# Performance work log

Hardware: AMD Instinct MI355X
Metric: run time of the kernel (lower is better)

Reference implementation:

```python
import jax, jax.numpy as jnp
import numpy as np

EPS = 1e-5  # torch GroupNorm default
KNN_K = 16


def _knn_idx(Q, P, K):
    # Q:[B,Nq,3], P:[B,Np,3] -> idx [B,Nq,K], ascending squared distance
    d = (jnp.sum(Q * Q, -1)[:, :, None] + jnp.sum(P * P, -1)[:, None, :]
         - 2.0 * jnp.einsum('bqc,bkc->bqk', Q, P))
    _, idx = jax.lax.top_k(-d, K)
    return idx


def _gather_nbr(feat_bnc, idx_bqk):
    # feat:[B,Np,C], idx:[B,Nq,K] -> [B,Nq,K,C]  (knn_gather)
    return jax.vmap(lambda f, i: f[i])(feat_bnc, idx_bqk)


def _group_norm(x_bcnk, gamma, beta, num_groups=8):
    B, C, N, K = x_bcnk.shape
    G = min(num_groups, C)
    xg = x_bcnk.reshape(B, G, C // G, N, K)
    mu = xg.mean(axis=(2, 3, 4), keepdims=True)
    var = xg.var(axis=(2, 3, 4), keepdims=True)
    xn = ((xg - mu) / jnp.sqrt(var + EPS)).reshape(B, C, N, K)
    return xn * gamma[None, :, None, None] + beta[None, :, None, None]


def _edge_conv(Fq_bcn, Fk_bcn, Pq_b3n, Pk_b3n, k, W, gamma, beta):
    # EdgeConv: concat(x_j - x_i, x_i) -> conv1x1 -> GN -> ReLU -> max over K
    idx = _knn_idx(Pq_b3n.transpose(0, 2, 1), Pk_b3n.transpose(0, 2, 1), k)
    nbr = _gather_nbr(Fk_bcn.transpose(0, 2, 1), idx)          # [B,Nq,K,Cin]
    Fi = jnp.broadcast_to(Fq_bcn.transpose(0, 2, 1)[:, :, None, :], nbr.shape)
    pair = jnp.concatenate([nbr - Fi, Fi], axis=-1)            # [B,Nq,K,2Cin]
    out = jnp.einsum('oc,bnkc->bonk', W, pair)                 # conv 1x1, no bias
    out = _group_norm(out, gamma, beta)
    out = jax.nn.relu(out)
    return out.max(axis=-1)                                    # [B,Cout,Nq]


def _fps_idx(P_b3n, m):
    # Farthest point sampling starting at index 0 (pytorch3d default)
    def one(Pn3):
        d0 = jnp.sum((Pn3 - Pn3[0]) ** 2, -1)
        def step(dists, _):
            nxt = jnp.argmax(dists)
            d = jnp.sum((Pn3 - Pn3[nxt]) ** 2, -1)
            return jnp.minimum(dists, d), nxt
        _, idxs = jax.lax.scan(step, d0, None, length=m - 1)
        return jnp.concatenate([jnp.zeros((1,), jnp.int32), idxs.astype(jnp.int32)])
    return jax.vmap(one)(P_b3n.transpose(0, 2, 1))


def _gather_bcn(x_bcn, idx_bm):
    return jax.vmap(lambda x, i: x[:, i])(x_bcn, idx_bm)


def setup_inputs() -> dict:
    key = jax.random.key(0)
    ks = jax.random.split(key, 8)
    B, N = 2, 8192
    def w(k, shape, s=0.1):
        return jax.random.normal(k, shape, jnp.float32) * s
    return {
        'xyz': jax.random.normal(ks[0], (B, 3, N), jnp.float32),
        'stem_w': w(ks[1], (8, 3)), 'stem_b': jnp.zeros((8,), jnp.float32),
        'w1': w(ks[2], (32, 16)),  'g1': jnp.ones((32,), jnp.float32),  'b1': jnp.zeros((32,), jnp.float32),
        'w2': w(ks[3], (64, 64)),  'g2': jnp.ones((64,), jnp.float32),  'b2': jnp.zeros((64,), jnp.float32),
        'w3': w(ks[4], (64, 128)), 'g3': jnp.ones((64,), jnp.float32),  'b3': jnp.zeros((64,), jnp.float32),
        'w4': w(ks[5], (128, 128)),'g4': jnp.ones((128,), jnp.float32), 'b4': jnp.zeros((128,), jnp.float32),
    }


def reference(xyz, stem_w, stem_b, w1, g1, b1, w2, g2, b2, w3, g3, b3, w4, g4, b4):
    K = KNN_K
    P0 = xyz                                                     # [B,3,N0]
    F0 = jnp.einsum('oc,bcn->bon', stem_w, xyz) + stem_b[None, :, None]
    F0a = _edge_conv(F0, F0, P0, P0, K, w1, g1, b1)              # [B,32,N0]
    N0 = P0.shape[2]
    N1 = max(1, N0 // 4)
    idx1 = _fps_idx(P0, N1)
    P1 = _gather_bcn(P0, idx1)
    F1sk = _gather_bcn(F0a, idx1)
    F1a = _edge_conv(F1sk, F0a, P1, P0, K, w2, g2, b2)           # [B,64,N1]
    N2 = max(1, N1 // 4)
    idx2 = _fps_idx(P1, N2)
    P2 = _gather_bcn(P1, idx2)
    F2sk = _gather_bcn(F1a, idx2)
    F2mid = _edge_conv(F2sk, F1a, P2, P1, K, w3, g3, b3)         # [B,64,N2]
    F2a = _edge_conv(F2mid, F1a, P2, P1, K, w4, g4, b4)          # [B,128,N2]
    return (P0, F0a, P1, F1a, P2, F2a)
```

## Files before the change

### kernel.cpp

```cpp
#include <hip/hip_runtime.h>
#include <math.h>

typedef unsigned long long ull;

__global__ __launch_bounds__(256) void stem_fused(const float* __restrict__ xyz,
    const float* __restrict__ w, const float* __restrict__ bias,
    float* __restrict__ F0, float* __restrict__ P0o, int N){
  int id = blockIdx.x*256 + threadIdx.x;
  int n = id % N; int b = id / N;
  float x = xyz[((size_t)b*3+0)*N+n];
  float y = xyz[((size_t)b*3+1)*N+n];
  float z = xyz[((size_t)b*3+2)*N+n];
  P0o[((size_t)b*3+0)*N+n] = x;
  P0o[((size_t)b*3+1)*N+n] = y;
  P0o[((size_t)b*3+2)*N+n] = z;
  #pragma unroll
  for (int o=0;o<8;o++){
    float v = fmaf(w[o*3+0],x, fmaf(w[o*3+1],y, fmaf(w[o*3+2],z, bias[o])));
    F0[((size_t)b*8+o)*N+n] = v;
  }
}

__global__ __launch_bounds__(256) void knn_fused(
    const float* __restrict__ Pq, const float* __restrict__ Pp,
    int* __restrict__ idxk, int Nq, int Np){
  __shared__ float4 tile[4][256];
  __shared__ float  pd[16][4][64];
  __shared__ int    pi[16][4][64];
  int t = threadIdx.x, w = t>>6, l = t&63;
  int b = blockIdx.y;
  int qn = blockIdx.x*64 + l;
  const float* Pqb = Pq + (size_t)b*3*Nq;
  const float* Ppb = Pp + (size_t)b*3*Np;
  float qx = Pqb[qn], qy = Pqb[Nq+qn], qz = Pqb[2*Nq+qn];
  float qq = __fadd_rn(__fadd_rn(__fmul_rn(qx,qx),__fmul_rn(qy,qy)),__fmul_rn(qz,qz));

  float dl[16]; int il[16];
  #pragma unroll
  for (int u=0;u<16;u++){ dl[u]=INFINITY; il[u]=-1; }
  float maxd = INFINITY; int maxslot = 0;

  int CANDS = Np >> 2;
  int c0 = w*CANDS;
  for (int tb=0; tb<CANDS; tb+=256){
    __syncthreads();
    #pragma unroll
    for (int k=0;k<4;k++){
      int p = c0 + tb + k*64 + l;
      float px = Ppb[p], py = Ppb[Np+p], pz = Ppb[2*Np+p];
      float pp = __fadd_rn(__fadd_rn(__fmul_rn(px,px),__fmul_rn(py,py)),__fmul_rn(pz,pz));
      tile[w][k*64+l] = make_float4(px,py,pz,pp);
    }
    __syncthreads();
    for (int j=0;j<256;j++){
      float4 c = tile[w][j];
      float dot = __fadd_rn(__fadd_rn(__fmul_rn(qx,c.x),__fmul_rn(qy,c.y)),__fmul_rn(qz,c.z));
      float dc  = __fsub_rn(__fadd_rn(qq,c.w), __fmul_rn(2.0f,dot));
      if (dc < maxd){
        int pidx = c0 + tb + j;
        #pragma unroll
        for (int u=0;u<16;u++){ bool sel=(maxslot==u); dl[u]=sel?dc:dl[u]; il[u]=sel?pidx:il[u]; }
        maxd = dl[0]; maxslot = 0;
        #pragma unroll
        for (int u=1;u<16;u++){ bool g=(dl[u]>maxd); maxd=g?dl[u]:maxd; maxslot=g?u:maxslot; }
      }
    }
  }
  #pragma unroll
  for (int u=0;u<16;u++){ pd[u][w][l]=dl[u]; pi[u][w][l]=il[u]; }
  __syncthreads();
  if (t < 64){
    int q = t;
    float mdl[16]; int mil[16];
    #pragma unroll
    for (int u=0;u<16;u++){ mdl[u]=INFINITY; mil[u]=0x7fffffff; }
    float mmaxd = INFINITY; int mmaxi = 0x7fffffff; int mslot = 0;
    for (int s=0;s<4;s++){
      #pragma unroll
      for (int u=0;u<16;u++){
        float d = pd[u][s][q]; int ii = pi[u][s][q];
        bool better = (d < mmaxd) || (d == mmaxd && ii < mmaxi);
        if (better){
          #pragma unroll
          for (int v=0;v<16;v++){ bool sel=(mslot==v); mdl[v]=sel?d:mdl[v]; mil[v]=sel?ii:mil[v]; }
          mmaxd = mdl[0]; mmaxi = mil[0]; mslot = 0;
          #pragma unroll
          for (int v=1;v<16;v++){
            bool g = (mdl[v]>mmaxd) || (mdl[v]==mmaxd && mil[v]>mmaxi);
            mmaxd=g?mdl[v]:mmaxd; mmaxi=g?mil[v]:mmaxi; mslot=g?v:mslot;
          }
        }
      }
    }
    #pragma unroll
    for (int u=0;u<16;u++)
      idxk[((size_t)b*Nq + blockIdx.x*64 + q)*16 + u] = mil[u];
  }
}

template<int CIN, int COUT>
__global__ __launch_bounds__(1024) void edge_conv_pre(
    const float* __restrict__ Fk, const float* __restrict__ Fi,
    const int* __restrict__ idx, const float* __restrict__ W,
    float* __restrict__ pre, float* __restrict__ partS,
    float* __restrict__ partQ, int pstride, int Nq, int Np){
  constexpr int C2  = 2*CIN;
  constexpr int PAD = C2 + 4;
  constexpr int TO  = (COUT <= 64) ? COUT : 64;
  constexpr int OP  = COUT / TO;
  constexpr int CPG = COUT/8;
  constexpr int WPG = CPG/4;
  extern __shared__ float sm[];
  float* Wl = sm;
  float* Pl = sm + COUT*PAD;
  int t = threadIdx.x;
  int n = blockIdx.x, b = blockIdx.y;
  for (int e=t; e<COUT*C2; e += blockDim.x){
    int o=e/C2, c=e%C2; Wl[o*PAD+c] = W[e];
  }
  const int* idxn = idx + ((size_t)b*Nq + n)*16;
  for (int e=t; e<16*C2; e += blockDim.x){
    int k = e/C2, c = e%C2;
    int cc = (c < CIN) ? c : (c-CIN);
    float fi = Fi[((size_t)b*CIN + cc)*Nq + n];
    float v;
    if (c < CIN){ int nb = idxn[k]; v = Fk[((size_t)b*CIN + c)*Np + nb] - fi; }
    else v = fi;
    Pl[k*PAD+c] = v;
  }
  __syncthreads();
  int k = t & 15, o0 = t >> 4;
  float accv[OP];
  #pragma unroll
  for (int op=0; op<OP; op++){
    int o = o0 + op*TO;
    float acc = 0.f;
    #pragma unroll
    for (int c=0;c<C2;c+=4){
      float4 wv = *(const float4*)&Wl[o*PAD+c];
      float4 pv = *(const float4*)&Pl[k*PAD+c];
      acc = fmaf(wv.x,pv.x,acc); acc = fmaf(wv.y,pv.y,acc);
      acc = fmaf(wv.z,pv.z,acc); acc = fmaf(wv.w,pv.w,acc);
    }
    accv[op] = acc;
    pre[(((size_t)b*COUT + o)*Nq + n)*16 + k] = acc;
  }
  int w = t>>6;
  #pragma unroll
  for (int op=0; op<OP; op++){
    float s1 = accv[op], s2 = accv[op]*accv[op];
    #pragma unroll
    for (int off=32; off>=1; off>>=1){ s1 += __shfl_down(s1,off); s2 += __shfl_down(s2,off); }
    if ((t&63)==0){
      int o = o0 + op*TO;
      int g = o / CPG;
      int slot = n*WPG + (w % WPG);
      partS[((size_t)(b*8+g))*pstride + slot] = s1;
      partQ[((size_t)(b*8+g))*pstride + slot] = s2;
    }
  }
}

__global__ __launch_bounds__(256) void gn_combine(const float* __restrict__ partS,
    const float* __restrict__ partQ, float2* __restrict__ stats,
    int nslot, int pstride, double cnt){
  int bg = blockIdx.x, t = threadIdx.x;
  const float* ps = partS + (size_t)bg*pstride;
  const float* pq = partQ + (size_t)bg*pstride;
  double s=0.0, q=0.0;
  for (int i=t; i<nslot; i+=256){ s += (double)ps[i]; q += (double)pq[i]; }
  #pragma unroll
  for (int off=32; off>=1; off>>=1){ s += __shfl_down(s,off); q += __shfl_down(q,off); }
  __shared__ double ls[4], lq[4];
  int wid = t>>6;
  if ((t&63)==0){ ls[wid]=s; lq[wid]=q; }
  __syncthreads();
  if (t==0){
    double S=ls[0]+ls[1]+ls[2]+ls[3], Q=lq[0]+lq[1]+lq[2]+lq[3];
    double mu = S/cnt;
    double var = Q/cnt - mu*mu;
    stats[bg] = make_float2((float)mu, (float)(1.0/sqrt(var+1e-5)));
  }
}

template<int COUT>
__global__ __launch_bounds__(256) void gn_apply(const float* __restrict__ pre,
    const float2* __restrict__ stats, const float* __restrict__ gamma,
    const float* __restrict__ beta, float* __restrict__ outF, int Nq){
  int id = blockIdx.x*256 + threadIdx.x;
  int o = (id/Nq)%COUT; int b = id/(Nq*COUT);
  int g = o/(COUT/8);
  float2 st = stats[b*8+g];
  float muf = st.x, rstd = st.y;
  float ga=gamma[o], be=beta[o];
  const float4* p = (const float4*)(pre + (size_t)id*16);
  float m = 0.f;
  #pragma unroll
  for (int q=0;q<4;q++){
    float4 v = p[q];
    m = fmaxf(m, fmaf((v.x-muf)*rstd, ga, be));
    m = fmaxf(m, fmaf((v.y-muf)*rstd, ga, be));
    m = fmaxf(m, fmaf((v.z-muf)*rstd, ga, be));
    m = fmaxf(m, fmaf((v.w-muf)*rstd, ga, be));
  }
  outF[id] = m;
}

template<int CTRL>
__device__ __forceinline__ float dpp_maxf(float x){
  int y = __builtin_amdgcn_update_dpp(0, __float_as_int(x), CTRL, 0xf, 0xf, true);
  return fmaxf(x, __int_as_float(y));
}

template<int PPT, int BLK, int M>
__global__ __launch_bounds__(BLK, 1) void fps_kernel(const float* __restrict__ P,
    int* __restrict__ idx_out){
  constexpr int N  = PPT*BLK;
  constexpr int NW = BLK/64;
  constexpr int Q  = PPT/4;
  extern __shared__ __align__(16) float sm[];
  float* lx = sm; float* ly = sm+N; float* lz = sm+2*N;
  ull* wk = (ull*)(sm + 3*N);
  int b = blockIdx.x, t = threadIdx.x;
  const float* Pb = P + (size_t)b*3*N;
  for (int i=t; i<N; i+=BLK){ lx[i]=Pb[i]; ly[i]=Pb[N+i]; lz[i]=Pb[2*N+i]; }
  __syncthreads();
  float px[PPT], py[PPT], pz[PPT], dist[PPT];
  #pragma unroll
  for (int j=0;j<PPT;j++){ int p=t*PPT+j; px[j]=lx[p]; py[j]=ly[p]; pz[j]=lz[p]; }
  #pragma unroll
  for (int j=0;j<PPT;j++){
    asm volatile("" : "+v"(px[j]), "+v"(py[j]), "+v"(pz[j]));
  }
  float sx = lx[0], sy = ly[0], sz = lz[0];
  float bd = -1.f; int bj = 0;
  #pragma unroll
  for (int j=0;j<PPT;j++){
    float dx=__fsub_rn(px[j],sx), dy=__fsub_rn(py[j],sy), dz=__fsub_rn(pz[j],sz);
    float dd=__fadd_rn(__fadd_rn(__fmul_rn(dx,dx),__fmul_rn(dy,dy)),__fmul_rn(dz,dz));
    dist[j]=dd;
    bool c = dd > bd; bd = c?dd:bd; bj = c?j:bj;
  }
  int pbest = t*PPT + bj;
  if (t==0) idx_out[(size_t)b*M] = 0;
  int wid = t>>6, lane = t&63, par = 0;
  for (int i=1;i<M;i++){
    float r = bd;
    r = dpp_maxf<0x111>(r); r = dpp_maxf<0x112>(r);
    r = dpp_maxf<0x114>(r); r = dpp_maxf<0x118>(r);
    r = dpp_maxf<0x142>(r); r = dpp_maxf<0x143>(r);
    float wmax = __int_as_float(__builtin_amdgcn_readlane(__float_as_int(r), 63));
    ull msk = __ballot(bd == wmax);
    int srcl = __ffsll(msk) - 1;
    int wp = __builtin_amdgcn_readlane(pbest, srcl);
    if (lane==0)
      wk[par*NW + wid] = ((ull)__float_as_uint(wmax)<<32)
                       | (unsigned)(~(unsigned)wp);
    __syncthreads();
    ull best = wk[par*NW];
    #pragma unroll
    for (int w=1;w<NW;w++){ ull o = wk[par*NW+w]; best = (o>best)?o:best; }
    unsigned widx = ~(unsigned)best;
    if (t==0) idx_out[(size_t)b*M + i] = (int)widx;
    float nsx = lx[widx], nsy = ly[widx], nsz = lz[widx];
    par ^= 1;
    float nb0=-1.f, nb1=-1.f, nb2=-1.f, nb3=-1.f;
    int   nj0=0,    nj1=0,    nj2=0,    nj3=0;
    #pragma unroll
    for (int j=0;j<PPT;j++){
      float dx=__fsub_rn(px[j],nsx), dy=__fsub_rn(py[j],nsy), dz=__fsub_rn(pz[j],nsz);
      float dd=__fadd_rn(__fadd_rn(__fmul_rn(dx,dx),__fmul_rn(dy,dy)),__fmul_rn(dz,dz));
      float nd = fminf(dist[j], dd);
      dist[j] = nd;
      if (j < Q)        { bool c = nd > nb0; nb0 = c?nd:nb0; nj0 = c?j:nj0; }
      else if (j < 2*Q) { bool c = nd > nb1; nb1 = c?nd:nb1; nj1 = c?j:nj1; }
      else if (j < 3*Q) { bool c = nd > nb2; nb2 = c?nd:nb2; nj2 = c?j:nj2; }
      else              { bool c = nd > nb3; nb3 = c?nd:nb3; nj3 = c?j:nj3; }
    }
    bool ca = nb1 > nb0; float ta = ca?nb1:nb0; int tja = ca?nj1:nj0;
    bool cb = nb3 > nb2; float tb = cb?nb3:nb2; int tjb = cb?nj3:nj2;
    bool cc = tb > ta;   bd = cc?tb:ta;         int nbj = cc?tjb:tja;
    pbest = t*PPT + nbj;
  }
}

__global__ __launch_bounds__(256) void gather_fused(float* __restrict__ Pdst,
    const float* __restrict__ Psrc, float* __restrict__ Fdst,
    const float* __restrict__ Fsrc, const int* __restrict__ idxv,
    int CF, int Nsrc, int M){
  int per = (3+CF)*M;
  int total = 2*per;
  for (int id = blockIdx.x*256 + threadIdx.x; id < total; id += gridDim.x*256){
    int b = id/per, r = id%per, c = r/M, m = r%M;
    int sn = idxv[(size_t)b*M + m];
    if (c < 3)
      Pdst[((size_t)b*3+c)*M+m] = Psrc[((size_t)b*3+c)*Nsrc+sn];
    else {
      int cf = c-3;
      Fdst[((size_t)b*CF+cf)*M+m] = Fsrc[((size_t)b*CF+cf)*Nsrc+sn];
    }
  }
}

extern "C" void kernel_launch(void* const* d_in, const int* in_sizes, int n_in,
                              void* d_out, int out_size, void* d_ws, size_t ws_size,
                              hipStream_t stream) {
  const float* xyz    = (const float*)d_in[0];
  const float* stem_w = (const float*)d_in[1];
  const float* stem_b = (const float*)d_in[2];
  const float* w1 = (const float*)d_in[3];
  const float* g1 = (const float*)d_in[4];
  const float* b1 = (const float*)d_in[5];
  const float* w2 = (const float*)d_in[6];
  const float* g2 = (const float*)d_in[7];
  const float* b2 = (const float*)d_in[8];
  const float* w3 = (const float*)d_in[9];
  const float* g3 = (const float*)d_in[10];
  const float* b3 = (const float*)d_in[11];
  const float* w4 = (const float*)d_in[12];
  const float* g4 = (const float*)d_in[13];
  const float* b4 = (const float*)d_in[14];

  float* out = (float*)d_out;
  float* P0o  = out + 0;
  float* F0a  = out + 49152;
  float* P1o  = out + 573440;
  float* F1a  = out + 585728;
  float* P2o  = out + 847872;
  float* F2a  = out + 850944;

  char* ws = (char*)d_ws;
  float* F0     = (float*)(ws + 0);
  float* pre    = (float*)(ws + 524288);
  int*   idxk   = (int*)  (ws + 34078720);
  float2* stats = (float2*)(ws + 35127296);
  int*   idx1   = (int*)  (ws + 35127424);
  int*   idx2   = (int*)  (ws + 35143808);
  float* F1sk   = (float*)(ws + 35147904);
  float* F2sk   = (float*)(ws + 35672192);
  float* F2mid  = (float*)(ws + 35934336);
  float* pS1 = (float*)(ws + 35147904);
  float* pQ1 = (float*)(ws + 35672192);
  float* pS2 = (float*)(ws + 17825792);
  float* pQ2 = (float*)(ws + 18087936);

  size_t smem_c1 = (size_t)(32*20  + 16*20 )*4;
  size_t smem_c2 = (size_t)(64*68  + 16*68 )*4;
  size_t smem_c3 = (size_t)(64*132 + 16*132)*4;
  size_t smem_c4 = (size_t)(128*132+ 16*132)*4;
  size_t smem_f1 = (size_t)3*8192*4 + 256;
  size_t smem_f2 = (size_t)3*2048*4 + 256;

  stem_fused<<<64, 256, 0, stream>>>(xyz, stem_w, stem_b, F0, P0o, 8192);
  knn_fused<<<dim3(128,2), 256, 0, stream>>>(xyz, xyz, idxk, 8192, 8192);
  edge_conv_pre<8,32><<<dim3(8192,2), 512, smem_c1, stream>>>(F0, F0, idxk, w1, pre, pS1, pQ1, 8192, 8192, 8192);
  gn_combine<<<16, 256, 0, stream>>>(pS1, pQ1, stats, 8192, 8192, 524288.0);
  gn_apply<32><<<2048, 256, 0, stream>>>(pre, stats, g1, b1, F0a, 8192);

  fps_kernel<32,256,2048><<<2, 256, smem_f1, stream>>>(xyz, idx1);
  gather_fused<<<560, 256, 0, stream>>>(P1o, xyz, F1sk, F0a, idx1, 32, 8192, 2048);

  knn_fused<<<dim3(32,2), 256, 0, stream>>>(P1o, xyz, idxk, 2048, 8192);
  edge_conv_pre<32,64><<<dim3(2048,2), 1024, smem_c2, stream>>>(F0a, F1sk, idxk, w2, pre, pS2, pQ2, 4096, 2048, 8192);
  gn_combine<<<16, 256, 0, stream>>>(pS2, pQ2, stats, 4096, 4096, 262144.0);
  gn_apply<64><<<1024, 256, 0, stream>>>(pre, stats, g2, b2, F1a, 2048);

  fps_kernel<8,256,512><<<2, 256, smem_f2, stream>>>(P1o, idx2);
  gather_fused<<<268, 256, 0, stream>>>(P2o, P1o, F2sk, F1a, idx2, 64, 2048, 512);

  knn_fused<<<dim3(8,2), 256, 0, stream>>>(P2o, P1o, idxk, 512, 2048);
  edge_conv_pre<64,64><<<dim3(512,2), 1024, smem_c3, stream>>>(F1a, F2sk, idxk, w3, pre, pS2, pQ2, 4096, 512, 2048);
  gn_combine<<<16, 256, 0, stream>>>(pS2, pQ2, stats, 1024, 4096, 65536.0);
  gn_apply<64><<<256, 256, 0, stream>>>(pre, stats, g3, b3, F2mid, 512);

  edge_conv_pre<64,128><<<dim3(512,2), 1024, smem_c4, stream>>>(F1a, F2mid, idxk, w4, pre, pS2, pQ2, 4096, 512, 2048);
  gn_combine<<<16, 256, 0, stream>>>(pS2, pQ2, stats, 2048, 4096, 131072.0);
  gn_apply<128><<<512, 256, 0, stream>>>(pre, stats, g4, b4, F2a, 512);

  (void)in_sizes; (void)n_in; (void)out_size; (void)ws_size;
}
```

Before: 3.490 ms.

## Widen FPS blocks to 512 threads and fuse small GroupNorm stages

FPS now runs with 512 threads per block and half the points per thread, using a single serial argmax chain instead of four interleaved ones. This shortens the per-thread latency of the serial FPS loop, at the cost of a wider cross-wave reduction. The last two GroupNorm combine+apply pairs are replaced by one kernel per group that recomputes the stats in double precision directly from the pre-activation buffer, which removes two launches per stage. The fused kernel runs only 16 blocks and ignores the partial sums edge_conv_pre still writes.

```diff
diff --git a/kernel.cpp b/kernel.cpp
--- a/kernel.cpp
+++ b/kernel.cpp
@@ -206,6 +206,61 @@
   outF[id] = m;
 }
 
+template<int COUT>
+__global__ __launch_bounds__(1024) void gn_fused(const float* __restrict__ pre,
+    const float* __restrict__ gamma, const float* __restrict__ beta,
+    float* __restrict__ outF, int Nq){
+  constexpr int CPG = COUT/8;
+  int g = blockIdx.x, b = blockIdx.y, t = threadIdx.x;
+  size_t base = (((size_t)b*COUT + g*CPG)*(size_t)Nq)*16;
+  const float* p = pre + base;
+  int len = CPG*Nq*16;
+  double s=0.0, sq=0.0;
+  for (int i = t*4; i < len; i += 4096){
+    float4 v = *(const float4*)(p+i);
+    s += (double)v.x; sq = fma((double)v.x,(double)v.x,sq);
+    s += (double)v.y; sq = fma((double)v.y,(double)v.y,sq);
+    s += (double)v.z; sq = fma((double)v.z,(double)v.z,sq);
+    s += (double)v.w; sq = fma((double)v.w,(double)v.w,sq);
+  }
+  #pragma unroll
+  for (int off=32; off>=1; off>>=1){ s += __shfl_down(s, off); sq += __shfl_down(sq, off); }
+  __shared__ double ls[16], lq[16];
+  __shared__ float stats[2];
+  int wid = t>>6;
+  if ((t&63)==0){ ls[wid]=s; lq[wid]=sq; }
+  __syncthreads();
+  if (t==0){
+    double S=0.0, Q=0.0;
+    #pragma unroll
+    for (int w=0;w<16;w++){ S+=ls[w]; Q+=lq[w]; }
+    double cnt = (double)CPG*(double)Nq*16.0;
+    double mu  = S/cnt;
+    double var = Q/cnt - mu*mu;
+    stats[0] = (float)mu;
+    stats[1] = (float)(1.0/sqrt(var+1e-5));
+  }
+  __syncthreads();
+  float muf = stats[0], rstd = stats[1];
+  int outs = CPG*Nq;
+  for (int e=t; e<outs; e+=1024){
+    int ol = e/Nq, n = e - ol*Nq;
+    int o = g*CPG + ol;
+    float ga = gamma[o], be = beta[o];
+    const float4* pp = (const float4*)(p + (size_t)e*16);
+    float m = 0.f;
+    #pragma unroll
+    for (int q=0;q<4;q++){
+      float4 v = pp[q];
+      m = fmaxf(m, fmaf((v.x-muf)*rstd, ga, be));
+      m = fmaxf(m, fmaf((v.y-muf)*rstd, ga, be));
+      m = fmaxf(m, fmaf((v.z-muf)*rstd, ga, be));
+      m = fmaxf(m, fmaf((v.w-muf)*rstd, ga, be));
+    }
+    outF[((size_t)b*COUT + o)*Nq + n] = m;
+  }
+}
+
 template<int CTRL>
 __device__ __forceinline__ float dpp_maxf(float x){
   int y = __builtin_amdgcn_update_dpp(0, __float_as_int(x), CTRL, 0xf, 0xf, true);
@@ -213,11 +268,10 @@
 }
 
 template<int PPT, int BLK, int M>
-__global__ __launch_bounds__(BLK, 1) void fps_kernel(const float* __restrict__ P,
+__global__ __launch_bounds__(BLK, 2) void fps_kernel(const float* __restrict__ P,
     int* __restrict__ idx_out){
   constexpr int N  = PPT*BLK;
   constexpr int NW = BLK/64;
-  constexpr int Q  = PPT/4;
   extern __shared__ __align__(16) float sm[];
   float* lx = sm; float* ly = sm+N; float* lz = sm+2*N;
   ull* wk = (ull*)(sm + 3*N);
@@ -264,23 +318,16 @@
     if (t==0) idx_out[(size_t)b*M + i] = (int)widx;
     float nsx = lx[widx], nsy = ly[widx], nsz = lz[widx];
     par ^= 1;
-    float nb0=-1.f, nb1=-1.f, nb2=-1.f, nb3=-1.f;
-    int   nj0=0,    nj1=0,    nj2=0,    nj3=0;
+    float nbd = -1.f; int nbj = 0;
     #pragma unroll
     for (int j=0;j<PPT;j++){
       float dx=__fsub_rn(px[j],nsx), dy=__fsub_rn(py[j],nsy), dz=__fsub_rn(pz[j],nsz);
       float dd=__fadd_rn(__fadd_rn(__fmul_rn(dx,dx),__fmul_rn(dy,dy)),__fmul_rn(dz,dz));
       float nd = fminf(dist[j], dd);
       dist[j] = nd;
-      if (j < Q)        { bool c = nd > nb0; nb0 = c?nd:nb0; nj0 = c?j:nj0; }
-      else if (j < 2*Q) { bool c = nd > nb1; nb1 = c?nd:nb1; nj1 = c?j:nj1; }
-      else if (j < 3*Q) { bool c = nd > nb2; nb2 = c?nd:nb2; nj2 = c?j:nj2; }
-      else              { bool c = nd > nb3; nb3 = c?nd:nb3; nj3 = c?j:nj3; }
-    }
-    bool ca = nb1 > nb0; float ta = ca?nb1:nb0; int tja = ca?nj1:nj0;
-    bool cb = nb3 > nb2; float tb = cb?nb3:nb2; int tjb = cb?nj3:nj2;
-    bool cc = tb > ta;   bd = cc?tb:ta;         int nbj = cc?tjb:tja;
-    pbest = t*PPT + nbj;
+      bool c = nd > nbd; nbd = c?nd:nbd; nbj = c?j:nbj;
+    }
+    bd = nbd; pbest = t*PPT + nbj;
   }
 }
 
@@ -357,7 +404,7 @@
   gn_combine<<<16, 256, 0, stream>>>(pS1, pQ1, stats, 8192, 8192, 524288.0);
   gn_apply<32><<<2048, 256, 0, stream>>>(pre, stats, g1, b1, F0a, 8192);
 
-  fps_kernel<32,256,2048><<<2, 256, smem_f1, stream>>>(xyz, idx1);
+  fps_kernel<16,512,2048><<<2, 512, smem_f1, stream>>>(xyz, idx1);
   gather_fused<<<560, 256, 0, stream>>>(P1o, xyz, F1sk, F0a, idx1, 32, 8192, 2048);
 
   knn_fused<<<dim3(32,2), 256, 0, stream>>>(P1o, xyz, idxk, 2048, 8192);
@@ -365,17 +412,15 @@
   gn_combine<<<16, 256, 0, stream>>>(pS2, pQ2, stats, 4096, 4096, 262144.0);
   gn_apply<64><<<1024, 256, 0, stream>>>(pre, stats, g2, b2, F1a, 2048);
 
-  fps_kernel<8,256,512><<<2, 256, smem_f2, stream>>>(P1o, idx2);
+  fps_kernel<4,512,512><<<2, 512, smem_f2, stream>>>(P1o, idx2);
   gather_fused<<<268, 256, 0, stream>>>(P2o, P1o, F2sk, F1a, idx2, 64, 2048, 512);
 
   knn_fused<<<dim3(8,2), 256, 0, stream>>>(P2o, P1o, idxk, 512, 2048);
   edge_conv_pre<64,64><<<dim3(512,2), 1024, smem_c3, stream>>>(F1a, F2sk, idxk, w3, pre, pS2, pQ2, 4096, 512, 2048);
-  gn_combine<<<16, 256, 0, stream>>>(pS2, pQ2, stats, 1024, 4096, 65536.0);
-  gn_apply<64><<<256, 256, 0, stream>>>(pre, stats, g3, b3, F2mid, 512);
+  gn_fused<64><<<dim3(8,2), 1024, 0, stream>>>(pre, g3, b3, F2mid, 512);
 
   edge_conv_pre<64,128><<<dim3(512,2), 1024, smem_c4, stream>>>(F1a, F2mid, idxk, w4, pre, pS2, pQ2, 4096, 512, 2048);
-  gn_combine<<<16, 256, 0, stream>>>(pS2, pQ2, stats, 2048, 4096, 131072.0);
-  gn_apply<128><<<512, 256, 0, stream>>>(pre, stats, g4, b4, F2a, 512);
+  gn_fused<128><<<dim3(8,2), 1024, 0, stream>>>(pre, g4, b4, F2a, 512);
 
   (void)in_sizes; (void)n_in; (void)out_size; (void)ws_size;
 }
```

Result: slower. 3.609 ms (+3.4%).
